# Optimization experiments

Measured on AMD Instinct MI355X. Metric: run time of the kernel, lower is better.

## Reference

```python
import jax, jax.numpy as jnp
import numpy as np

H = 1024      # hidden_size
I = 4096      # intermediate_size
E = 8         # num_experts
TOP_K = 2
LB_COEF = 0.01


def setup_inputs() -> dict:
    key = jax.random.key(0)
    ks = jax.random.split(key, 8)
    s_h = 1.0 / np.sqrt(H)
    s_i = 1.0 / np.sqrt(I)
    return {
        "x": jax.random.normal(ks[0], (2, 2048, H), dtype=jnp.float32),
        "Wr": jax.random.normal(ks[1], (H, E), dtype=jnp.float32) * s_h,
        "br": jnp.zeros((E,), dtype=jnp.float32),
        "W1": jax.random.normal(ks[2], (E, H, I), dtype=jnp.float32) * s_h,
        "b1": jnp.zeros((E, I), dtype=jnp.float32),
        "W2": jax.random.normal(ks[3], (E, I, H), dtype=jnp.float32) * s_i,
        "b2": jnp.zeros((E, H), dtype=jnp.float32),
    }


def _moe_forward(x, Wr, br, W1, b1, W2, b2):
    B, S, Hd = x.shape
    x_flat = x.reshape(-1, Hd)                      # [T, H]
    T = x_flat.shape[0]

    # ---- Router: softmax probs, top-k, renormalize ----
    logits = x_flat @ Wr + br                       # [T, E]
    probs = jax.nn.softmax(logits, axis=-1)         # [T, E]
    topk_w, topk_idx = jax.lax.top_k(probs, TOP_K)  # [T, K]
    topk_w = topk_w / jnp.sum(topk_w, axis=-1, keepdims=True)

    # ---- Load-balance aux loss (switch-style) ----
    onehot = jax.nn.one_hot(topk_idx, E, dtype=x.dtype)   # [T, K, E]
    frac_tokens = onehot.mean(axis=(0, 1))                 # [E]
    frac_probs = probs.mean(axis=0)                        # [E]
    aux_loss = E * jnp.sum(frac_tokens * frac_probs) * LB_COEF

    # combine_weights[t, e] = routing weight of expert e for token t (0 if unselected)
    combine = jnp.sum(topk_w[..., None] * onehot, axis=1)  # [T, E]

    # ---- Experts: dense per-expert FFN, weighted combine ----
    out = jnp.zeros_like(x_flat)
    for e in range(E):
        h = jax.nn.gelu(x_flat @ W1[e] + b1[e])            # [T, I]
        y = h @ W2[e] + b2[e]                              # [T, H]
        out = out + y * combine[:, e:e + 1]
    return out.reshape(B, S, Hd), aux_loss


def reference(x, Wr, br, W1, b1, W2, b2):
    return _moe_forward(x, Wr, br, W1, b1, W2, b2)
```

## Files before the change

### kernel.cpp

```cpp
#include <hip/hip_runtime.h>
#include <hip/hip_bf16.h>

#define HD 1024
#define ID 4096
#define NE 8
#define NT 4096
#define NSLOT (NT*2)

typedef __attribute__((ext_vector_type(4))) float f32x4;
typedef __attribute__((ext_vector_type(8))) short bf16x8;
typedef __attribute__((ext_vector_type(4))) unsigned int u32x4;
typedef __attribute__((ext_vector_type(2))) unsigned int u32x2;
typedef unsigned short u16;

__device__ __forceinline__ u16 f2b(float f) {
  __hip_bfloat16 h = __float2bfloat16(f);
  return __builtin_bit_cast(unsigned short, h);
}
__device__ __forceinline__ unsigned int pack2(float a, float b) {
  return (unsigned int)f2b(a) | ((unsigned int)f2b(b) << 16);
}
__device__ __forceinline__ void gload16(const void* g, void* l) {
  __builtin_amdgcn_global_load_lds(
      (const __attribute__((address_space(1))) unsigned int*)g,
      (__attribute__((address_space(3))) unsigned int*)l, 16, 0, 0);
}
__device__ __forceinline__ float gelu_tanh(float v) {
  float c = v + 0.044715f * v * v * v;
  float u = 1.5957691216057308f * c;
  float t = 1.0f - 2.0f / (__expf(u) + 1.0f);
  return 0.5f * v * (1.0f + t);
}

__global__ __launch_bounds__(256) void k_transpose2(
    const float* __restrict__ W1, u16* __restrict__ w1t,
    const float* __restrict__ W2, u16* __restrict__ w2t) {
  __shared__ float tile[64][65];
  int id = blockIdx.x;
  const float* src;
  u16* dst;
  int R, C, e, rem;
  if (id < 8192) {
    e = id >> 10; rem = id & 1023;
    src = W1; dst = w1t; R = HD; C = ID;
  } else {
    id -= 8192;
    e = id >> 10; rem = id & 1023;
    src = W2; dst = w2t; R = ID; C = HD;
  }
  int ctiles = C >> 6;
  int c0 = (rem % ctiles) * 64;
  int r0 = (rem / ctiles) * 64;
  int t = threadIdx.x;
  const float* s = src + (size_t)e * R * C;
#pragma unroll
  for (int i = 0; i < 16; ++i) {
    int r = i * 4 + (t >> 6);
    tile[r][t & 63] = s[(size_t)(r0 + r) * C + c0 + (t & 63)];
  }
  __syncthreads();
  u16* d = dst + (size_t)e * R * C;
#pragma unroll
  for (int i = 0; i < 4; ++i) {
    int c = i * 16 + (t >> 4);
    int rb = (t & 15) * 4;
    u32x2 p;
    p[0] = pack2(tile[rb + 0][c], tile[rb + 1][c]);
    p[1] = pack2(tile[rb + 2][c], tile[rb + 3][c]);
    *(u32x2*)&d[(size_t)(c0 + c) * R + r0 + rb] = p;
  }
}

__global__ __launch_bounds__(256) void k_router(
    const float* __restrict__ x, const float* __restrict__ Wr,
    const float* __restrict__ br, int* __restrict__ cnt,
    int* __restrict__ slotE, int* __restrict__ slotLoc,
    float* __restrict__ slotW, float* __restrict__ psumG,
    u16* __restrict__ xb) {
  __shared__ float wrt[NE * HD];
  __shared__ float blkp[NE];
  int t = threadIdx.x;
  if (t < NE) blkp[t] = 0.0f;
  for (int i = t; i < NE * HD; i += 256) wrt[(i & 7) * HD + (i >> 3)] = Wr[i];
  __syncthreads();
  int wave = t >> 6, lane = t & 63;
  int token = blockIdx.x * 4 + wave;
  const float* xr = x + (size_t)token * HD;
  u16* xbr = xb + (size_t)token * HD;
  float acc[NE] = {0, 0, 0, 0, 0, 0, 0, 0};
#pragma unroll 4
  for (int j = 0; j < 16; ++j) {
    int h = j * 64 + lane;
    float xv = xr[h];
    xbr[h] = f2b(xv);
#pragma unroll
    for (int e = 0; e < NE; ++e) acc[e] += xv * wrt[e * HD + h];
  }
#pragma unroll
  for (int d = 1; d < 64; d <<= 1) {
#pragma unroll
    for (int e = 0; e < NE; ++e) acc[e] += __shfl_xor(acc[e], d, 64);
  }
  if (lane == 0) {
    float lg[NE], p[NE];
    float m = -1e30f;
#pragma unroll
    for (int e = 0; e < NE; ++e) { lg[e] = acc[e] + br[e]; m = fmaxf(m, lg[e]); }
    float s = 0.f;
#pragma unroll
    for (int e = 0; e < NE; ++e) { p[e] = expf(lg[e] - m); s += p[e]; }
    float inv = 1.0f / s;
    int i1 = 0, i2 = -1;
    float v1 = -1.f, v2 = -1.f;
#pragma unroll
    for (int e = 0; e < NE; ++e) {
      p[e] *= inv;
      atomicAdd(&blkp[e], p[e]);
      if (p[e] > v1) { v2 = v1; i2 = i1; v1 = p[e]; i1 = e; }
      else if (p[e] > v2) { v2 = p[e]; i2 = e; }
    }
    float wsum = v1 + v2;
    int l1 = atomicAdd(&cnt[i1], 1);
    int l2 = atomicAdd(&cnt[i2], 1);
    slotE[token * 2] = i1;     slotLoc[token * 2] = l1;     slotW[token * 2] = v1 / wsum;
    slotE[token * 2 + 1] = i2; slotLoc[token * 2 + 1] = l2; slotW[token * 2 + 1] = v2 / wsum;
  }
  __syncthreads();
  if (t < NE) atomicAdd(&psumG[t], blkp[t]);
}

__global__ void k_finalize(const float* __restrict__ psumG, const int* __restrict__ cnt,
                           int* __restrict__ off, float* __restrict__ out_aux) {
  if (threadIdx.x == 0) {
    int o = 0;
    float a = 0.f;
    for (int e = 0; e < NE; ++e) {
      off[e] = o;
      o += cnt[e];
      a += ((float)cnt[e] / (float)NSLOT) * (psumG[e] / (float)NT);
    }
    off[NE] = o;
    out_aux[0] = (float)NE * a * 0.01f;
  }
}

__global__ void k_scatter(const int* __restrict__ slotE, const int* __restrict__ slotLoc,
                          const float* __restrict__ slotW, const int* __restrict__ off,
                          int* __restrict__ rowTok, float* __restrict__ rowW) {
  int i = blockIdx.x * 256 + threadIdx.x;
  int pos = off[slotE[i]] + slotLoc[i];
  if (pos < 0) pos = 0;
  if (pos >= NSLOT) pos = NSLOT - 1;
  rowTok[pos] = i >> 1;
  rowW[pos] = slotW[i];
}

#define STG(bf) do { \
    gload16(srcA0, &As[bf][c0 * 8]); \
    gload16(srcA1, &As[bf][c1 * 8]); \
    gload16(srcB0, &Bs[bf][c0 * 8]); \
    gload16(srcB1, &Bs[bf][c1 * 8]); \
    srcA0 += 32; srcA1 += 32; srcB0 += 32; srcB1 += 32; \
  } while (0)

__global__ __launch_bounds__(256, 3) void k_gemm1(
    const u16* __restrict__ xb, const u16* __restrict__ w1t,
    const float* __restrict__ b1, u16* __restrict__ hbuf,
    const int* __restrict__ cnt, const int* __restrict__ off,
    const int* __restrict__ rowTok) {
  const int NWG = NE * 32 * 32;
  int bid = blockIdx.x;
  int wg = (bid & 7) * (NWG / 8) + (bid >> 3);
  int e = wg >> 10;
  int rem = wg & 1023;
  int n0 = (rem >> 5) * 128;
  int m0 = (rem & 31) * 128;
  int ce = cnt[e];
  if (m0 >= ce) return;
  int oe = off[e];
  __shared__ u16 As[3][128 * 32];
  __shared__ u16 Bs[3][128 * 32];
  __shared__ int rtok[128];
  int t = threadIdx.x;
  if (t < 128) {
    int r = m0 + t;
    if (r >= ce) r = ce - 1;
    int tok = rowTok[oe + r];
    rtok[t] = (tok < 0) ? 0 : (tok >= NT ? NT - 1 : tok);
  }
  __syncthreads();
  int c0 = t, c1 = t + 256;
  int js0 = (c0 & 3) ^ ((c0 >> 3) & 3);
  int js1 = (c1 & 3) ^ ((c1 >> 3) & 3);
  const u16* srcA0 = xb + (size_t)rtok[c0 >> 2] * HD + js0 * 8;
  const u16* srcA1 = xb + (size_t)rtok[c1 >> 2] * HD + js1 * 8;
  const u16* bb = w1t + (size_t)e * ID * HD + (size_t)n0 * HD;
  const u16* srcB0 = bb + (size_t)(c0 >> 2) * HD + js0 * 8;
  const u16* srcB1 = bb + (size_t)(c1 >> 2) * HD + js1 * 8;
  int wave = t >> 6, lane = t & 63;
  int wr = wave >> 1, wc = wave & 1;
  int arow = wr * 64 + (lane & 15);
  int aoff = arow * 32 + ((lane >> 4) ^ ((arow >> 1) & 3)) * 8;
  int brow = wc * 64 + (lane & 15);
  int boff = brow * 32 + ((lane >> 4) ^ ((brow >> 1) & 3)) * 8;
  f32x4 acc[4][4] = {};
  const int NK = HD / 32;
  STG(0);
  STG(1);
  int rb = 0;
  for (int kt = 0; kt < NK; ++kt) {
    if (kt + 1 < NK) asm volatile("s_waitcnt vmcnt(4)" ::: "memory");
    else             asm volatile("s_waitcnt vmcnt(0)" ::: "memory");
    __builtin_amdgcn_s_barrier();
    const u16* ap = &As[rb][aoff];
    const u16* bp = &Bs[rb][boff];
    bf16x8 af[4], bfr[4];
#pragma unroll
    for (int m = 0; m < 4; ++m) af[m] = *(const bf16x8*)(ap + m * 16 * 32);
#pragma unroll
    for (int n = 0; n < 4; ++n) bfr[n] = *(const bf16x8*)(bp + n * 16 * 32);
#pragma unroll
    for (int m = 0; m < 4; ++m)
#pragma unroll
      for (int n = 0; n < 4; ++n)
        acc[m][n] = __builtin_amdgcn_mfma_f32_16x16x32_bf16(af[m], bfr[n], acc[m][n], 0, 0, 0);
    if (kt + 2 < NK) {
      int sb = rb + 2; if (sb >= 3) sb -= 3;
      STG(sb);
    }
    rb = (rb == 2) ? 0 : rb + 1;
  }
  const float* b1e = b1 + (size_t)e * ID + n0;
#pragma unroll
  for (int n = 0; n < 4; ++n) {
    int col = wc * 64 + n * 16 + (lane & 15);
    float bias = b1e[col];
#pragma unroll
    for (int m = 0; m < 4; ++m) {
      int rbase = wr * 64 + m * 16 + (lane >> 4) * 4;
#pragma unroll
      for (int r = 0; r < 4; ++r) {
        int grow = m0 + rbase + r;
        if (grow < ce) {
          float v = acc[m][n][r] + bias;
          hbuf[(size_t)(oe + grow) * ID + n0 + col] = f2b(gelu_tanh(v));
        }
      }
    }
  }
}

__global__ __launch_bounds__(256, 3) void k_gemm2(
    const u16* __restrict__ hbuf, const u16* __restrict__ w2t,
    const float* __restrict__ b2, float* __restrict__ out,
    const int* __restrict__ cnt, const int* __restrict__ off,
    const int* __restrict__ rowTok, const float* __restrict__ rowW) {
  const int NWG = NE * 32 * 2 * 8;
  int bid = blockIdx.x;
  int wg = (bid & 7) * (NWG / 8) + (bid >> 3);
  int e = wg >> 9;
  int rem = wg & 511;
  int ks = rem >> 8;
  int n0 = ((rem >> 5) & 7) * 128;
  int m0 = (rem & 31) * 128;
  int ce = cnt[e];
  if (m0 >= ce) return;
  int oe = off[e];
  int k0 = ks * (ID / 2);
  __shared__ u16 As[3][128 * 32];
  __shared__ u16 Bs[3][128 * 32];
  __shared__ int rtok[128];
  __shared__ float rw[128];
  int t = threadIdx.x;
  if (t < 128) {
    int r = m0 + t;
    int rc = (r < ce) ? r : ce - 1;
    int tok = rowTok[oe + rc];
    rtok[t] = (tok < 0) ? 0 : (tok >= NT ? NT - 1 : tok);
    rw[t] = (r < ce) ? rowW[oe + r] : 0.0f;
  }
  __syncthreads();
  int c0 = t, c1 = t + 256;
  int js0 = (c0 & 3) ^ ((c0 >> 3) & 3);
  int js1 = (c1 & 3) ^ ((c1 >> 3) & 3);
  int rA0 = m0 + (c0 >> 2); if (rA0 >= ce) rA0 = ce - 1;
  int rA1 = m0 + (c1 >> 2); if (rA1 >= ce) rA1 = ce - 1;
  const u16* srcA0 = hbuf + (size_t)(oe + rA0) * ID + k0 + js0 * 8;
  const u16* srcA1 = hbuf + (size_t)(oe + rA1) * ID + k0 + js1 * 8;
  const u16* bb = w2t + (size_t)e * HD * ID + (size_t)n0 * ID + k0;
  const u16* srcB0 = bb + (size_t)(c0 >> 2) * ID + js0 * 8;
  const u16* srcB1 = bb + (size_t)(c1 >> 2) * ID + js1 * 8;
  int wave = t >> 6, lane = t & 63;
  int wr = wave >> 1, wc = wave & 1;
  int arow = wr * 64 + (lane & 15);
  int aoff = arow * 32 + ((lane >> 4) ^ ((arow >> 1) & 3)) * 8;
  int brow = wc * 64 + (lane & 15);
  int boff = brow * 32 + ((lane >> 4) ^ ((brow >> 1) & 3)) * 8;
  f32x4 acc[4][4] = {};
  const int NK = (ID / 2) / 32;
  STG(0);
  STG(1);
  int rb = 0;
  for (int kt = 0; kt < NK; ++kt) {
    if (kt + 1 < NK) asm volatile("s_waitcnt vmcnt(4)" ::: "memory");
    else             asm volatile("s_waitcnt vmcnt(0)" ::: "memory");
    __builtin_amdgcn_s_barrier();
    const u16* ap = &As[rb][aoff];
    const u16* bp = &Bs[rb][boff];
    bf16x8 af[4], bfr[4];
#pragma unroll
    for (int m = 0; m < 4; ++m) af[m] = *(const bf16x8*)(ap + m * 16 * 32);
#pragma unroll
    for (int n = 0; n < 4; ++n) bfr[n] = *(const bf16x8*)(bp + n * 16 * 32);
#pragma unroll
    for (int m = 0; m < 4; ++m)
#pragma unroll
      for (int n = 0; n < 4; ++n)
        acc[m][n] = __builtin_amdgcn_mfma_f32_16x16x32_bf16(af[m], bfr[n], acc[m][n], 0, 0, 0);
    if (kt + 2 < NK) {
      int sb = rb + 2; if (sb >= 3) sb -= 3;
      STG(sb);
    }
    rb = (rb == 2) ? 0 : rb + 1;
  }
  const float* b2e = b2 + (size_t)e * HD + n0;
#pragma unroll
  for (int n = 0; n < 4; ++n) {
    int col = wc * 64 + n * 16 + (lane & 15);
    float bias = (ks == 0) ? b2e[col] : 0.0f;
#pragma unroll
    for (int m = 0; m < 4; ++m) {
      int rbase = wr * 64 + m * 16 + (lane >> 4) * 4;
#pragma unroll
      for (int r = 0; r < 4; ++r) {
        int grow = m0 + rbase + r;
        if (grow < ce) {
          float v = (acc[m][n][r] + bias) * rw[rbase + r];
          atomicAdd(&out[(size_t)rtok[rbase + r] * HD + n0 + col], v);
        }
      }
    }
  }
}

extern "C" void kernel_launch(void* const* d_in, const int* in_sizes, int n_in,
                              void* d_out, int out_size, void* d_ws, size_t ws_size,
                              hipStream_t stream) {
  const float* x  = (const float*)d_in[0];
  const float* Wr = (const float*)d_in[1];
  const float* br = (const float*)d_in[2];
  const float* W1 = (const float*)d_in[3];
  const float* b1 = (const float*)d_in[4];
  const float* W2 = (const float*)d_in[5];
  const float* b2 = (const float*)d_in[6];
  float* out = (float*)d_out;

  char* ws = (char*)d_ws;
  size_t o = 0;
  auto alloc = [&](size_t bytes) {
    void* p = ws + o;
    o = (o + bytes + 255) & ~(size_t)255;
    return p;
  };
  u16* xb    = (u16*)alloc((size_t)NT * HD * 2);
  u16* w1t   = (u16*)alloc((size_t)NE * ID * HD * 2);
  u16* w2t   = (u16*)alloc((size_t)NE * ID * HD * 2);
  u16* hbuf  = (u16*)alloc((size_t)NSLOT * ID * 2);
  int* cnt     = (int*)alloc(NE * 4);
  float* psumG = (float*)alloc(NE * 4);
  int* off     = (int*)alloc(16 * 4);
  int* slotE   = (int*)alloc(NSLOT * 4);
  int* slotLoc = (int*)alloc(NSLOT * 4);
  float* slotW = (float*)alloc(NSLOT * 4);
  int* rowTok  = (int*)alloc(NSLOT * 4);
  float* rowW  = (float*)alloc(NSLOT * 4);

  if (ws_size < o) return;

  (void)hipMemsetAsync(cnt, 0, NE * 4, stream);
  (void)hipMemsetAsync(psumG, 0, NE * 4, stream);
  (void)hipMemsetAsync(out, 0, (size_t)out_size * 4, stream);
  k_transpose2<<<16384, 256, 0, stream>>>(W1, w1t, W2, w2t);
  k_router<<<NT / 4, 256, 0, stream>>>(x, Wr, br, cnt, slotE, slotLoc, slotW, psumG, xb);
  k_finalize<<<1, 64, 0, stream>>>(psumG, cnt, off, out + (size_t)NT * HD);
  k_scatter<<<NSLOT / 256, 256, 0, stream>>>(slotE, slotLoc, slotW, off, rowTok, rowW);
  k_gemm1<<<NE * 32 * 32, 256, 0, stream>>>(xb, w1t, b1, hbuf, cnt, off, rowTok);
  k_gemm2<<<NE * 32 * 2 * 8, 256, 0, stream>>>(hbuf, w2t, b2, out, cnt, off, rowTok, rowW);
}
```

Baseline: 519.6 us.

## Load B operand directly into registers, bypassing LDS, with register double-buffering

Both expert GEMM kernels stop staging the weight (B) tiles through shared memory. Each wave now loads its own MFMA B fragments from global memory straight into registers, double-buffered one k-step ahead, while A still goes through the triple-buffered LDS pipeline. This halves LDS usage, so launch bounds rise to 4 blocks per SM. The trade-off is that waves sharing a column block each fetch the same B data, which doubles B global and cache traffic, and the compiler-inserted waits on the register loads may expose latency.

Result: slower. 743.7 us (+43.1%).

```diff
diff --git a/kernel.cpp b/kernel.cpp
--- a/kernel.cpp
+++ b/kernel.cpp
@@ -155,15 +155,41 @@
   rowW[pos] = slotW[i];
 }
 
-#define STG(bf) do { \
+#define STGA(bf) do { \
     gload16(srcA0, &As[bf][c0 * 8]); \
     gload16(srcA1, &As[bf][c1 * 8]); \
-    gload16(srcB0, &Bs[bf][c0 * 8]); \
-    gload16(srcB1, &Bs[bf][c1 * 8]); \
-    srcA0 += 32; srcA1 += 32; srcB0 += 32; srcB1 += 32; \
+    srcA0 += 32; srcA1 += 32; \
   } while (0)
 
-__global__ __launch_bounds__(256, 3) void k_gemm1(
+#define LOADB(dst, ktv) do { \
+    size_t kb_ = (size_t)(ktv) * 32 + kfrag; \
+    dst[0] = *(const bf16x8*)(bbl0 + kb_); \
+    dst[1] = *(const bf16x8*)(bbl1 + kb_); \
+    dst[2] = *(const bf16x8*)(bbl2 + kb_); \
+    dst[3] = *(const bf16x8*)(bbl3 + kb_); \
+  } while (0)
+
+#define KSTEP(kt, cur, nxt, NKV) do { \
+    if ((kt) + 1 < (NKV)) asm volatile("s_waitcnt vmcnt(6)" ::: "memory"); \
+    else                  asm volatile("s_waitcnt vmcnt(0)" ::: "memory"); \
+    __builtin_amdgcn_s_barrier(); \
+    const u16* ap = &As[rb][aoff]; \
+    bf16x8 af[4]; \
+    _Pragma("unroll") for (int m = 0; m < 4; ++m) \
+      af[m] = *(const bf16x8*)(ap + m * 16 * 32); \
+    int ktn = ((kt) + 1 < (NKV)) ? (kt) + 1 : (NKV) - 1; \
+    LOADB(nxt, ktn); \
+    _Pragma("unroll") for (int m = 0; m < 4; ++m) \
+      _Pragma("unroll") for (int n = 0; n < 4; ++n) \
+        acc[m][n] = __builtin_amdgcn_mfma_f32_16x16x32_bf16(af[m], cur[n], acc[m][n], 0, 0, 0); \
+    if ((kt) + 2 < (NKV)) { \
+      int sb = rb + 2; if (sb >= 3) sb -= 3; \
+      STGA(sb); \
+    } \
+    rb = (rb == 2) ? 0 : rb + 1; \
+  } while (0)
+
+__global__ __launch_bounds__(256, 4) void k_gemm1(
     const u16* __restrict__ xb, const u16* __restrict__ w1t,
     const float* __restrict__ b1, u16* __restrict__ hbuf,
     const int* __restrict__ cnt, const int* __restrict__ off,
@@ -179,7 +205,6 @@
   if (m0 >= ce) return;
   int oe = off[e];
   __shared__ u16 As[3][128 * 32];
-  __shared__ u16 Bs[3][128 * 32];
   __shared__ int rtok[128];
   int t = threadIdx.x;
   if (t < 128) {
@@ -194,41 +219,26 @@
   int js1 = (c1 & 3) ^ ((c1 >> 3) & 3);
   const u16* srcA0 = xb + (size_t)rtok[c0 >> 2] * HD + js0 * 8;
   const u16* srcA1 = xb + (size_t)rtok[c1 >> 2] * HD + js1 * 8;
-  const u16* bb = w1t + (size_t)e * ID * HD + (size_t)n0 * HD;
-  const u16* srcB0 = bb + (size_t)(c0 >> 2) * HD + js0 * 8;
-  const u16* srcB1 = bb + (size_t)(c1 >> 2) * HD + js1 * 8;
   int wave = t >> 6, lane = t & 63;
   int wr = wave >> 1, wc = wave & 1;
   int arow = wr * 64 + (lane & 15);
   int aoff = arow * 32 + ((lane >> 4) ^ ((arow >> 1) & 3)) * 8;
-  int brow = wc * 64 + (lane & 15);
-  int boff = brow * 32 + ((lane >> 4) ^ ((brow >> 1) & 3)) * 8;
+  size_t kfrag = (size_t)(lane >> 4) * 8;
+  const u16* bbase = w1t + (size_t)e * ID * HD;
+  const u16* bbl0 = bbase + (size_t)(n0 + wc * 64 + 0 * 16 + (lane & 15)) * HD;
+  const u16* bbl1 = bbase + (size_t)(n0 + wc * 64 + 1 * 16 + (lane & 15)) * HD;
+  const u16* bbl2 = bbase + (size_t)(n0 + wc * 64 + 2 * 16 + (lane & 15)) * HD;
+  const u16* bbl3 = bbase + (size_t)(n0 + wc * 64 + 3 * 16 + (lane & 15)) * HD;
   f32x4 acc[4][4] = {};
   const int NK = HD / 32;
-  STG(0);
-  STG(1);
+  bf16x8 bvA[4], bvB[4];
+  STGA(0);
+  STGA(1);
+  LOADB(bvA, 0);
   int rb = 0;
-  for (int kt = 0; kt < NK; ++kt) {
-    if (kt + 1 < NK) asm volatile("s_waitcnt vmcnt(4)" ::: "memory");
-    else             asm volatile("s_waitcnt vmcnt(0)" ::: "memory");
-    __builtin_amdgcn_s_barrier();
-    const u16* ap = &As[rb][aoff];
-    const u16* bp = &Bs[rb][boff];
-    bf16x8 af[4], bfr[4];
-#pragma unroll
-    for (int m = 0; m < 4; ++m) af[m] = *(const bf16x8*)(ap + m * 16 * 32);
-#pragma unroll
-    for (int n = 0; n < 4; ++n) bfr[n] = *(const bf16x8*)(bp + n * 16 * 32);
-#pragma unroll
-    for (int m = 0; m < 4; ++m)
-#pragma unroll
-      for (int n = 0; n < 4; ++n)
-        acc[m][n] = __builtin_amdgcn_mfma_f32_16x16x32_bf16(af[m], bfr[n], acc[m][n], 0, 0, 0);
-    if (kt + 2 < NK) {
-      int sb = rb + 2; if (sb >= 3) sb -= 3;
-      STG(sb);
-    }
-    rb = (rb == 2) ? 0 : rb + 1;
+  for (int k2 = 0; k2 < NK; k2 += 2) {
+    KSTEP(k2,     bvA, bvB, NK);
+    KSTEP(k2 + 1, bvB, bvA, NK);
   }
   const float* b1e = b1 + (size_t)e * ID + n0;
 #pragma unroll
@@ -250,7 +260,7 @@
   }
 }
 
-__global__ __launch_bounds__(256, 3) void k_gemm2(
+__global__ __launch_bounds__(256, 4) void k_gemm2(
     const u16* __restrict__ hbuf, const u16* __restrict__ w2t,
     const float* __restrict__ b2, float* __restrict__ out,
     const int* __restrict__ cnt, const int* __restrict__ off,
@@ -268,7 +278,6 @@
   int oe = off[e];
   int k0 = ks * (ID / 2);
   __shared__ u16 As[3][128 * 32];
-  __shared__ u16 Bs[3][128 * 32];
   __shared__ int rtok[128];
   __shared__ float rw[128];
   int t = threadIdx.x;
@@ -287,41 +296,26 @@
   int rA1 = m0 + (c1 >> 2); if (rA1 >= ce) rA1 = ce - 1;
   const u16* srcA0 = hbuf + (size_t)(oe + rA0) * ID + k0 + js0 * 8;
   const u16* srcA1 = hbuf + (size_t)(oe + rA1) * ID + k0 + js1 * 8;
-  const u16* bb = w2t + (size_t)e * HD * ID + (size_t)n0 * ID + k0;
-  const u16* srcB0 = bb + (size_t)(c0 >> 2) * ID + js0 * 8;
-  const u16* srcB1 = bb + (size_t)(c1 >> 2) * ID + js1 * 8;
   int wave = t >> 6, lane = t & 63;
   int wr = wave >> 1, wc = wave & 1;
   int arow = wr * 64 + (lane & 15);
   int aoff = arow * 32 + ((lane >> 4) ^ ((arow >> 1) & 3)) * 8;
-  int brow = wc * 64 + (lane & 15);
-  int boff = brow * 32 + ((lane >> 4) ^ ((brow >> 1) & 3)) * 8;
+  size_t kfrag = (size_t)(lane >> 4) * 8;
+  const u16* bbase = w2t + (size_t)e * HD * ID + k0;
+  const u16* bbl0 = bbase + (size_t)(n0 + wc * 64 + 0 * 16 + (lane & 15)) * ID;
+  const u16* bbl1 = bbase + (size_t)(n0 + wc * 64 + 1 * 16 + (lane & 15)) * ID;
+  const u16* bbl2 = bbase + (size_t)(n0 + wc * 64 + 2 * 16 + (lane & 15)) * ID;
+  const u16* bbl3 = bbase + (size_t)(n0 + wc * 64 + 3 * 16 + (lane & 15)) * ID;
   f32x4 acc[4][4] = {};
   const int NK = (ID / 2) / 32;
-  STG(0);
-  STG(1);
+  bf16x8 bvA[4], bvB[4];
+  STGA(0);
+  STGA(1);
+  LOADB(bvA, 0);
   int rb = 0;
-  for (int kt = 0; kt < NK; ++kt) {
-    if (kt + 1 < NK) asm volatile("s_waitcnt vmcnt(4)" ::: "memory");
-    else             asm volatile("s_waitcnt vmcnt(0)" ::: "memory");
-    __builtin_amdgcn_s_barrier();
-    const u16* ap = &As[rb][aoff];
-    const u16* bp = &Bs[rb][boff];
-    bf16x8 af[4], bfr[4];
-#pragma unroll
-    for (int m = 0; m < 4; ++m) af[m] = *(const bf16x8*)(ap + m * 16 * 32);
-#pragma unroll
-    for (int n = 0; n < 4; ++n) bfr[n] = *(const bf16x8*)(bp + n * 16 * 32);
-#pragma unroll
-    for (int m = 0; m < 4; ++m)
-#pragma unroll
-      for (int n = 0; n < 4; ++n)
-        acc[m][n] = __builtin_amdgcn_mfma_f32_16x16x32_bf16(af[m], bfr[n], acc[m][n], 0, 0, 0);
-    if (kt + 2 < NK) {
-      int sb = rb + 2; if (sb >= 3) sb -= 3;
-      STG(sb);
-    }
-    rb = (rb == 2) ? 0 : rb + 1;
+  for (int k2 = 0; k2 < NK; k2 += 2) {
+    KSTEP(k2,     bvA, bvB, NK);
+    KSTEP(k2 + 1, bvB, bvA, NK);
   }
   const float* b2e = b2 + (size_t)e * HD + n0;
 #pragma unroll
```
